# Optimization experiments

Hardware: AMD Instinct MI355X
Metric: run time of the kernel (lower is better)

## Reference

```python
import jax, jax.numpy as jnp
import numpy as np

N_FFT = 2048
STRIDE = 512
PAD = N_FFT // 2  # center padding removed at the end
B = 4
T = 512  # number of spectrogram frames


def _make_kernels():
    n = np.arange(N_FFT)
    # ang[out_sample, freq_bin] = 2*pi*n*k/N  (create_fourier_kernels, freq_scale='no', freq_bins=n_fft)
    ang = 2.0 * np.pi * np.outer(n, n) / N_FFT
    kernel_cos = np.cos(ang).astype(np.float32)
    kernel_sin = np.sin(ang).astype(np.float32)
    # scipy.signal.get_window('hann', N, fftbins=True) -> periodic hann
    window = (0.5 - 0.5 * np.cos(2.0 * np.pi * n / N_FFT)).astype(np.float32)
    return kernel_cos, kernel_sin, window


def setup_inputs() -> dict:
    key = jax.random.key(0)
    X = jax.random.normal(key, (B, N_FFT, T, 2), dtype=jnp.float32)
    kc, ks, w = _make_kernels()
    return {
        "X": X,
        "kernel_cos": jnp.asarray(kc),
        "kernel_sin": jnp.asarray(ks),
        "window": jnp.asarray(w),
    }


def reference(X, kernel_cos, kernel_sin, window):
    # X: (B, n_fft, T, 2) complex spectrogram (onesided=False)
    b, n_fft, t, _ = X.shape
    Xr = X[..., 0]
    Xi = X[..., 1]
    # inverse DFT via dense matmul against sinusoidal kernels (conv2d in torch):
    # frames[b, n, t] = sum_f Xr[b,f,t]*cos(2pi n f/N) - Xi[b,f,t]*sin(2pi n f/N)
    frames = (jnp.einsum('bft,nf->bnt', Xr, kernel_cos)
              - jnp.einsum('bft,nf->bnt', Xi, kernel_sin))
    frames = frames * window[None, :, None] / n_fft
    # overlap-add (torch fold): out[b, t*stride + n] += frames[b, n, t]
    out_len = n_fft + STRIDE * (t - 1)
    idx = (jnp.arange(n_fft)[:, None] + STRIDE * jnp.arange(t)[None, :]).reshape(-1)
    y = jnp.zeros((b, out_len), frames.dtype).at[:, idx].add(frames.reshape(b, -1))
    # window sum-square normalization (torch_window_sumsquare)
    w_sq = jnp.broadcast_to((window * window)[:, None], (n_fft, t)).reshape(-1)
    w_sum = jnp.zeros((out_len,), window.dtype).at[idx].add(w_sq)
    nonzero = w_sum > 1e-10
    denom = jnp.where(nonzero, w_sum, jnp.ones_like(w_sum))
    y = jnp.where(nonzero[None, :], y / denom[None, :], y)
    # center=True, length=None -> trim pad_amount from both ends
    return y[:, PAD:-PAD]
```

## Files before the change

### kernel.cpp

```cpp
#include <hip/hip_runtime.h>

#define NFFT 2048
#define TT   512
#define BB   4
#define OUTL 261632

__device__ __forceinline__ int TIDX(int i, int c) {
    return i * 8 + ((c + i + (i >> 3)) & 7);
}

__device__ __forceinline__ float2 cmul(float2 a, float2 w) {
    return make_float2(a.x * w.x - a.y * w.y, a.x * w.y + a.y * w.x);
}

__device__ __forceinline__ void dft8(const float2 a[8], float2 o[8]) {
    float e0r = a[0].x + a[4].x, e0i = a[0].y + a[4].y;
    float e1r = a[0].x - a[4].x, e1i = a[0].y - a[4].y;
    float e2r = a[2].x + a[6].x, e2i = a[2].y + a[6].y;
    float e3r = a[6].y - a[2].y, e3i = a[2].x - a[6].x;
    float E0r = e0r + e2r, E0i = e0i + e2i;
    float E1r = e1r + e3r, E1i = e1i + e3i;
    float E2r = e0r - e2r, E2i = e0i - e2i;
    float E3r = e1r - e3r, E3i = e1i - e3i;
    float f0r = a[1].x + a[5].x, f0i = a[1].y + a[5].y;
    float f1r = a[1].x - a[5].x, f1i = a[1].y - a[5].y;
    float f2r = a[3].x + a[7].x, f2i = a[3].y + a[7].y;
    float f3r = a[7].y - a[3].y, f3i = a[3].x - a[7].x;
    float O0r = f0r + f2r, O0i = f0i + f2i;
    float O1r = f1r + f3r, O1i = f1i + f3i;
    float O2r = f0r - f2r, O2i = f0i - f2i;
    float O3r = f1r - f3r, O3i = f1i - f3i;
    const float h = 0.70710678118654752f;
    float W1r = h * (O1r - O1i), W1i = h * (O1r + O1i);
    float W2r = -O2i,            W2i = O2r;
    float W3r = -h * (O3r + O3i), W3i = h * (O3r - O3i);
    o[0] = make_float2(E0r + O0r, E0i + O0i);
    o[1] = make_float2(E1r + W1r, E1i + W1i);
    o[2] = make_float2(E2r + W2r, E2i + W2i);
    o[3] = make_float2(E3r + W3r, E3i + W3i);
    o[4] = make_float2(E0r - O0r, E0i - O0i);
    o[5] = make_float2(E1r - W1r, E1i - W1i);
    o[6] = make_float2(E2r - W2r, E2i - W2i);
    o[7] = make_float2(E3r - W3r, E3i - W3i);
}

__device__ __forceinline__ void twpow8(float2 o[8], float2 w1) {
    float2 w2 = cmul(w1, w1);
    float2 w3 = cmul(w2, w1);
    float2 w4 = cmul(w2, w2);
    o[1] = cmul(o[1], w1);
    o[2] = cmul(o[2], w2);
    o[3] = cmul(o[3], w3);
    o[4] = cmul(o[4], w4);
    o[5] = cmul(o[5], cmul(w4, w1));
    o[6] = cmul(o[6], cmul(w4, w2));
    o[7] = cmul(o[7], cmul(w4, w3));
}

__global__ __launch_bounds__(1024) void istft_k(const float* __restrict__ X,
                                                const float* __restrict__ kc,
                                                const float* __restrict__ ks,
                                                const float* __restrict__ win,
                                                float* __restrict__ out) {
    __shared__ float2 tile[2048 * 8];
    __shared__ float2 tw256[256];

    const int S  = blockIdx.x;
    const int c0 = S * 8;
    const int b  = c0 >> 9;
    const int t0 = c0 & 511;
    const int tid = threadIdx.x;

    if (tid < 256)
        tw256[tid] = make_float2(kc[2048 + tid], ks[2048 + tid]);

    const float* Xb = X + ((size_t)b * 2048 * 512 + t0) * 2;
    #pragma unroll
    for (int m = 0; m < 8; m++) {
        int f = m * 256 + (tid >> 2);
        int c = (tid & 3) * 2;
        const float4 v = *reinterpret_cast<const float4*>(Xb + ((size_t)f * 512 + c) * 2);
        tile[TIDX(f, c)]     = make_float2(v.x, v.y);
        tile[TIDX(f, c + 1)] = make_float2(v.z, v.w);
    }
    __syncthreads();

    const int g = tid >> 8;
    const int u = tid & 255;
    #pragma unroll 1
    for (int r = 0; r < 2; r++) {
        const int c = r * 4 + g;
        float2 a[8], o[8];
        #pragma unroll
        for (int l = 0; l < 8; l++) a[l] = tile[TIDX(u + 256 * l, c)];
        __syncthreads();
        dft8(a, o);
        twpow8(o, tw256[u]);
        #pragma unroll
        for (int k = 0; k < 8; k++) tile[TIDX(8 * u + k, c)] = o[k];
        __syncthreads();
        #pragma unroll
        for (int l = 0; l < 8; l++) a[l] = tile[TIDX(u + 256 * l, c)];
        __syncthreads();
        dft8(a, o);
        twpow8(o, tw256[u & ~7]);
        {
            int base = 64 * (u >> 3) + (u & 7);
            #pragma unroll
            for (int k = 0; k < 8; k++) tile[TIDX(base + 8 * k, c)] = o[k];
        }
        __syncthreads();
        #pragma unroll
        for (int l = 0; l < 8; l++) a[l] = tile[TIDX(u + 256 * l, c)];
        __syncthreads();
        dft8(a, o);
        twpow8(o, tw256[u & ~63]);
        {
            int base = 512 * (u >> 6) + (u & 63);
            #pragma unroll
            for (int k = 0; k < 8; k++) tile[TIDX(base + 64 * k, c)] = o[k];
        }
        __syncthreads();
        #pragma unroll
        for (int half = 0; half < 2; half++) {
            int uu = u + 256 * half;
            float2 d0 = tile[TIDX(uu, c)];
            float2 d1 = tile[TIDX(uu + 512, c)];
            float2 d2 = tile[TIDX(uu + 1024, c)];
            float2 d3 = tile[TIDX(uu + 1536, c)];
            float p0 = d0.x + d2.x;
            float p1 = d0.x - d2.x;
            float p2 = d1.x + d3.x;
            float p3 = d3.y - d1.y;
            tile[TIDX(uu, c)].x        = (p0 + p2) * win[uu];
            tile[TIDX(uu + 512, c)].x  = (p1 + p3) * win[uu + 512];
            tile[TIDX(uu + 1024, c)].x = (p0 - p2) * win[uu + 1024];
            tile[TIDX(uu + 1536, c)].x = (p1 - p3) * win[uu + 1536];
        }
    }
    __syncthreads();

    #pragma unroll
    for (int q = 0; q < 6; q++) {
        int idx = tid + 1024 * q;
        if (q >= 4 && idx - 4096 >= 1536) break;
        int jl = idx;
        int tb_l = jl >> 9;
        int rr = jl & 511;
        int tglob = t0 + tb_l;
        float sum = 0.f, ws = 0.f;
        #pragma unroll
        for (int k = 0; k < 4; k++) {
            int t = tglob - k;
            int n = rr + (k << 9);
            if (t >= 0 && t < TT) {
                float w = win[n];
                ws += w * w;
                int m = tb_l - k;
                if (m >= 0 && m < 8) sum += tile[TIDX(n, m)].x;
            }
        }
        float y = sum * (1.0f / 2048.0f);
        if (ws > 1e-10f) y /= ws;
        int jp = t0 * 512 + jl - 1024;
        if (jp >= 0 && jp < OUTL) {
            float* dst = out + (size_t)b * OUTL + jp;
            if (jl >= 1536 && jl < 4096) *dst = y;
            else                         atomicAdd(dst, y);
        }
    }
}

extern "C" void kernel_launch(void* const* d_in, const int* in_sizes, int n_in,
                              void* d_out, int out_size, void* d_ws, size_t ws_size,
                              hipStream_t stream) {
    const float* X  = (const float*)d_in[0];
    const float* kc = (const float*)d_in[1];
    const float* ks = (const float*)d_in[2];
    const float* w  = (const float*)d_in[3];
    float* out = (float*)d_out;

    hipMemsetAsync(out, 0, (size_t)out_size * sizeof(float), stream);
    istft_k<<<dim3(BB * TT / 8), dim3(1024), 0, stream>>>(X, kc, ks, w, out);
}
```

Measured before the change: 32.57 us.

## Halve frames per block and process two frames per thread with float4 tiles

Each block now handles 4 frames with 512 threads instead of 8 frames with 1024 threads, which halves LDS use to 64KB so more blocks fit per CU. Each thread runs two interleaved radix-8 FFT columns held in a float4 LDS layout with a new swizzle, so it issues wider LDS accesses and gains ILP from the two independent FFTs. Block indices are remapped to spread neighbouring frames across blocks. The trade-off is that overlap-add boundaries now cover a larger share of output, so more outputs go through atomicAdd instead of direct stores.

```diff
diff --git a/kernel.cpp b/kernel.cpp
--- a/kernel.cpp
+++ b/kernel.cpp
@@ -5,8 +5,8 @@
 #define BB   4
 #define OUTL 261632
 
-__device__ __forceinline__ int TIDX(int i, int c) {
-    return i * 8 + ((c + i + (i >> 3)) & 7);
+__device__ __forceinline__ int T4(int i, int sp) {
+    return ((i >> 1) << 2) | ((2 * (i & 1) + sp + (i >> 1) + (i >> 3)) & 3);
 }
 
 __device__ __forceinline__ float2 cmul(float2 a, float2 w) {
@@ -57,94 +57,114 @@
     o[7] = cmul(o[7], cmul(w4, w3));
 }
 
-__global__ __launch_bounds__(1024) void istft_k(const float* __restrict__ X,
-                                                const float* __restrict__ kc,
-                                                const float* __restrict__ ks,
-                                                const float* __restrict__ win,
-                                                float* __restrict__ out) {
-    __shared__ float2 tile[2048 * 8];
-    __shared__ float2 tw256[256];
+__global__ __launch_bounds__(512, 4) void istft_k(const float* __restrict__ X,
+                                                  const float* __restrict__ kc,
+                                                  const float* __restrict__ ks,
+                                                  const float* __restrict__ win,
+                                                  float* __restrict__ out) {
+    __shared__ float4 tile[4096];
+    __shared__ float2 tw[256];
 
     const int S  = blockIdx.x;
-    const int c0 = S * 8;
+    const int L  = ((S & 7) << 6) | (S >> 3);
+    const int c0 = L * 4;
     const int b  = c0 >> 9;
     const int t0 = c0 & 511;
     const int tid = threadIdx.x;
 
     if (tid < 256)
-        tw256[tid] = make_float2(kc[2048 + tid], ks[2048 + tid]);
+        tw[tid] = make_float2(kc[2048 + tid], ks[2048 + tid]);
 
     const float* Xb = X + ((size_t)b * 2048 * 512 + t0) * 2;
     #pragma unroll
     for (int m = 0; m < 8; m++) {
-        int f = m * 256 + (tid >> 2);
-        int c = (tid & 3) * 2;
-        const float4 v = *reinterpret_cast<const float4*>(Xb + ((size_t)f * 512 + c) * 2);
-        tile[TIDX(f, c)]     = make_float2(v.x, v.y);
-        tile[TIDX(f, c + 1)] = make_float2(v.z, v.w);
+        int f  = m * 256 + (tid >> 1);
+        int sp = tid & 1;
+        float4 v = *reinterpret_cast<const float4*>(Xb + (size_t)f * 1024 + sp * 4);
+        tile[T4(f, sp)] = v;
     }
     __syncthreads();
 
     const int g = tid >> 8;
     const int u = tid & 255;
+
+    float4 a4[8];
+    float2 x0[8], x1[8], o0[8], o1[8];
+
+    #pragma unroll
+    for (int l = 0; l < 8; l++) a4[l] = tile[T4(u + 256 * l, g)];
+    __syncthreads();
+    #pragma unroll
+    for (int l = 0; l < 8; l++) {
+        x0[l] = make_float2(a4[l].x, a4[l].y);
+        x1[l] = make_float2(a4[l].z, a4[l].w);
+    }
+    dft8(x0, o0); twpow8(o0, tw[u]);
+    dft8(x1, o1); twpow8(o1, tw[u]);
+    #pragma unroll
+    for (int k = 0; k < 8; k++)
+        tile[T4(8 * u + k, g)] = make_float4(o0[k].x, o0[k].y, o1[k].x, o1[k].y);
+    __syncthreads();
+
+    #pragma unroll
+    for (int l = 0; l < 8; l++) a4[l] = tile[T4(u + 256 * l, g)];
+    __syncthreads();
+    #pragma unroll
+    for (int l = 0; l < 8; l++) {
+        x0[l] = make_float2(a4[l].x, a4[l].y);
+        x1[l] = make_float2(a4[l].z, a4[l].w);
+    }
+    dft8(x0, o0); twpow8(o0, tw[u & ~7]);
+    dft8(x1, o1); twpow8(o1, tw[u & ~7]);
+    {
+        int base = 64 * (u >> 3) + (u & 7);
+        #pragma unroll
+        for (int k = 0; k < 8; k++)
+            tile[T4(base + 8 * k, g)] = make_float4(o0[k].x, o0[k].y, o1[k].x, o1[k].y);
+    }
+    __syncthreads();
+
+    #pragma unroll
+    for (int l = 0; l < 8; l++) a4[l] = tile[T4(u + 256 * l, g)];
+    __syncthreads();
+    #pragma unroll
+    for (int l = 0; l < 8; l++) {
+        x0[l] = make_float2(a4[l].x, a4[l].y);
+        x1[l] = make_float2(a4[l].z, a4[l].w);
+    }
+    dft8(x0, o0); twpow8(o0, tw[u & ~63]);
+    dft8(x1, o1); twpow8(o1, tw[u & ~63]);
+    {
+        int base = 512 * (u >> 6) + (u & 63);
+        #pragma unroll
+        for (int k = 0; k < 8; k++)
+            tile[T4(base + 64 * k, g)] = make_float4(o0[k].x, o0[k].y, o1[k].x, o1[k].y);
+    }
+    __syncthreads();
+
+    #pragma unroll
+    for (int half = 0; half < 2; half++) {
+        int uu = u + 256 * half;
+        float4 d0 = tile[T4(uu, g)];
+        float4 d1 = tile[T4(uu + 512, g)];
+        float4 d2 = tile[T4(uu + 1024, g)];
+        float4 d3 = tile[T4(uu + 1536, g)];
+        float p0 = d0.x + d2.x, p1 = d0.x - d2.x;
+        float p2 = d1.x + d3.x, p3 = d3.y - d1.y;
+        float q0 = d0.z + d2.z, q1 = d0.z - d2.z;
+        float q2 = d1.z + d3.z, q3 = d3.w - d1.w;
+        float w0 = win[uu], w1 = win[uu + 512], w2 = win[uu + 1024], w3 = win[uu + 1536];
+        tile[T4(uu, g)]        = make_float4((p0 + p2) * w0, 0.f, (q0 + q2) * w0, 0.f);
+        tile[T4(uu + 512, g)]  = make_float4((p1 + p3) * w1, 0.f, (q1 + q3) * w1, 0.f);
+        tile[T4(uu + 1024, g)] = make_float4((p0 - p2) * w2, 0.f, (q0 - q2) * w2, 0.f);
+        tile[T4(uu + 1536, g)] = make_float4((p1 - p3) * w3, 0.f, (q1 - q3) * w3, 0.f);
+    }
+    __syncthreads();
+
+    const float* tf = (const float*)tile;
     #pragma unroll 1
-    for (int r = 0; r < 2; r++) {
-        const int c = r * 4 + g;
-        float2 a[8], o[8];
-        #pragma unroll
-        for (int l = 0; l < 8; l++) a[l] = tile[TIDX(u + 256 * l, c)];
-        __syncthreads();
-        dft8(a, o);
-        twpow8(o, tw256[u]);
-        #pragma unroll
-        for (int k = 0; k < 8; k++) tile[TIDX(8 * u + k, c)] = o[k];
-        __syncthreads();
-        #pragma unroll
-        for (int l = 0; l < 8; l++) a[l] = tile[TIDX(u + 256 * l, c)];
-        __syncthreads();
-        dft8(a, o);
-        twpow8(o, tw256[u & ~7]);
-        {
-            int base = 64 * (u >> 3) + (u & 7);
-            #pragma unroll
-            for (int k = 0; k < 8; k++) tile[TIDX(base + 8 * k, c)] = o[k];
-        }
-        __syncthreads();
-        #pragma unroll
-        for (int l = 0; l < 8; l++) a[l] = tile[TIDX(u + 256 * l, c)];
-        __syncthreads();
-        dft8(a, o);
-        twpow8(o, tw256[u & ~63]);
-        {
-            int base = 512 * (u >> 6) + (u & 63);
-            #pragma unroll
-            for (int k = 0; k < 8; k++) tile[TIDX(base + 64 * k, c)] = o[k];
-        }
-        __syncthreads();
-        #pragma unroll
-        for (int half = 0; half < 2; half++) {
-            int uu = u + 256 * half;
-            float2 d0 = tile[TIDX(uu, c)];
-            float2 d1 = tile[TIDX(uu + 512, c)];
-            float2 d2 = tile[TIDX(uu + 1024, c)];
-            float2 d3 = tile[TIDX(uu + 1536, c)];
-            float p0 = d0.x + d2.x;
-            float p1 = d0.x - d2.x;
-            float p2 = d1.x + d3.x;
-            float p3 = d3.y - d1.y;
-            tile[TIDX(uu, c)].x        = (p0 + p2) * win[uu];
-            tile[TIDX(uu + 512, c)].x  = (p1 + p3) * win[uu + 512];
-            tile[TIDX(uu + 1024, c)].x = (p0 - p2) * win[uu + 1024];
-            tile[TIDX(uu + 1536, c)].x = (p1 - p3) * win[uu + 1536];
-        }
-    }
-    __syncthreads();
-
-    #pragma unroll
-    for (int q = 0; q < 6; q++) {
-        int idx = tid + 1024 * q;
-        if (q >= 4 && idx - 4096 >= 1536) break;
-        int jl = idx;
+    for (int q = 0; q < 7; q++) {
+        int jl = tid + 512 * q;
         int tb_l = jl >> 9;
         int rr = jl & 511;
         int tglob = t0 + tb_l;
@@ -157,7 +177,8 @@
                 float w = win[n];
                 ws += w * w;
                 int m = tb_l - k;
-                if (m >= 0 && m < 8) sum += tile[TIDX(n, m)].x;
+                if (m >= 0 && m < 4)
+                    sum += tf[T4(n, m >> 1) * 4 + (m & 1) * 2];
             }
         }
         float y = sum * (1.0f / 2048.0f);
@@ -165,7 +186,7 @@
         int jp = t0 * 512 + jl - 1024;
         if (jp >= 0 && jp < OUTL) {
             float* dst = out + (size_t)b * OUTL + jp;
-            if (jl >= 1536 && jl < 4096) *dst = y;
+            if (jl >= 1536 && jl < 2048) *dst = y;
             else                         atomicAdd(dst, y);
         }
     }
@@ -181,5 +202,5 @@
     float* out = (float*)d_out;
 
     hipMemsetAsync(out, 0, (size_t)out_size * sizeof(float), stream);
-    istft_k<<<dim3(BB * TT / 8), dim3(1024), 0, stream>>>(X, kc, ks, w, out);
-}
+    istft_k<<<dim3(BB * TT / 4), dim3(512), 0, stream>>>(X, kc, ks, w, out);
+}
```

After: 29.15 us. -10.5%, faster.
